# Kernel tuning notes

Hardware: AMD Instinct MI355X
Metric: run time of the kernel (lower is better)

## Reference

```python
import math
import jax, jax.numpy as jnp
import numpy as np

B, S, H, D = 8, 2048, 16, 80
DM = H * D  # 1280 = input_dims


def setup_inputs() -> dict:
    key = jax.random.key(0)
    ks = jax.random.split(key, 10)
    s = 0.02
    return {
        "x": jax.random.normal(ks[0], (B, S, DM), dtype=jnp.float32),
        "Wq": jax.random.normal(ks[1], (DM, DM), dtype=jnp.float32) * s,
        "bq": jnp.zeros((DM,), dtype=jnp.float32),
        "Wk": jax.random.normal(ks[2], (DM, DM), dtype=jnp.float32) * s,
        "bk": jnp.zeros((DM,), dtype=jnp.float32),
        "Wv": jax.random.normal(ks[3], (DM, DM), dtype=jnp.float32) * s,
        "bv": jnp.zeros((DM,), dtype=jnp.float32),
        "Wp": jax.random.normal(ks[4], (DM, DM), dtype=jnp.float32) * s,
        "bp": jnp.zeros((DM,), dtype=jnp.float32),
        "per_dim_scale": jnp.ones((D,), dtype=jnp.float32),
    }


def reference(x, Wq, bq, Wk, bk, Wv, bv, Wp, bp, per_dim_scale):
    # Projections: [B,S,DM] -> [B,S,H,D]
    q = (x @ Wq + bq).reshape(B, S, H, D)
    k = (x @ Wk + bk).reshape(B, S, H, D)
    v = (x @ Wv + bv).reshape(B, S, H, D)
    # Faithful to source: matmul over last two dims of (B,S,H,D) tensors,
    # i.e. scores are [B,S,H,H] -- mixing across HEADS at each position.
    scale = 1.0 / math.sqrt(D)
    attn = jnp.einsum('bshd,bstd->bsht', q, k) * scale  # [B,S,H,H]
    attn = jax.nn.softmax(attn, axis=-1)
    out = jnp.einsum('bsht,bstd->bshd', attn, v)  # [B,S,H,D]
    out = out * per_dim_scale  # broadcast over D
    out = out.reshape(B, S, DM)
    return out @ Wp + bp
```

## Files before the change

kernel.cpp:

```cpp
#include <hip/hip_runtime.h>
#include <hip/hip_bf16.h>

#define M_TOT   16384
#define DMODEL  1280
#define NHEAD   16
#define DHEAD   80
#define NTC     5
#define BK      64
#define NKT     (DMODEL / BK)

typedef __attribute__((ext_vector_type(8))) __bf16 bf16x8;
typedef __attribute__((ext_vector_type(4))) float  f32x4;

__device__ __forceinline__ void gload16(const void* g, void* l) {
  __builtin_amdgcn_global_load_lds(
      (const __attribute__((address_space(1))) void*)g,
      (__attribute__((address_space(3))) void*)l, 16, 0, 0);
}

__device__ __forceinline__ float bf2f(unsigned short u) {
  return __uint_as_float((unsigned)u << 16);
}

__global__ __launch_bounds__(256) void cvt_bf16_kernel(
    const float* __restrict__ x, __hip_bfloat16* __restrict__ y, int n4) {
  int i = blockIdx.x * 256 + threadIdx.x;
  if (i >= n4) return;
  float4 v = ((const float4*)x)[i];
  union { ushort4 u; __hip_bfloat16 h[4]; } o;
  o.h[0] = __float2bfloat16(v.x);
  o.h[1] = __float2bfloat16(v.y);
  o.h[2] = __float2bfloat16(v.z);
  o.h[3] = __float2bfloat16(v.w);
  ((ushort4*)y)[i] = o.u;
}

__global__ __launch_bounds__(256) void transpose_cvt_kernel(
    const float* __restrict__ W0, const float* __restrict__ W1,
    const float* __restrict__ W2, const float* __restrict__ W3,
    __hip_bfloat16* __restrict__ T0, __hip_bfloat16* __restrict__ T1,
    __hip_bfloat16* __restrict__ T2, __hip_bfloat16* __restrict__ T3) {
  const float* W = blockIdx.z == 0 ? W0 : blockIdx.z == 1 ? W1
                 : blockIdx.z == 2 ? W2 : W3;
  __hip_bfloat16* T = blockIdx.z == 0 ? T0 : blockIdx.z == 1 ? T1
                    : blockIdx.z == 2 ? T2 : T3;
  __shared__ float tile[32][33];
  int bx = blockIdx.x * 32, by = blockIdx.y * 32;
  int tx = threadIdx.x, ty = threadIdx.y;
  for (int j = 0; j < 32; j += 8)
    tile[ty + j][tx] = W[(size_t)(by + ty + j) * DMODEL + bx + tx];
  __syncthreads();
  for (int j = 0; j < 32; j += 8)
    T[(size_t)(bx + ty + j) * DMODEL + by + tx] = __float2bfloat16(tile[tx][ty + j]);
}

#define MFMA16(AF, BF, MB)                                                   \
  do {                                                                       \
    _Pragma("unroll")                                                        \
    for (int j_ = 0; j_ < 4; ++j_) {                                         \
      _Pragma("unroll")                                                      \
      for (int n_ = 0; n_ < 4; ++n_)                                         \
        acc[(MB) + j_][n_] = __builtin_amdgcn_mfma_f32_16x16x32_bf16(        \
            AF[j_], BF[n_], acc[(MB) + j_][n_], 0, 0, 0);                    \
    }                                                                        \
  } while (0)

template <bool OUT_BF16>
__global__ __launch_bounds__(512, 2) void gemm_bt_kernel(
    const __hip_bfloat16* __restrict__ A,
    const __hip_bfloat16* __restrict__ Bt0,
    const __hip_bfloat16* __restrict__ Bt1,
    const __hip_bfloat16* __restrict__ Bt2,
    const float* __restrict__ bias0, const float* __restrict__ bias1,
    const float* __restrict__ bias2,
    void* __restrict__ C0, void* __restrict__ C1, void* __restrict__ C2) {
  const int mat   = blockIdx.y / NTC;
  const int ntile = blockIdx.y % NTC;
  const __hip_bfloat16* Bt = mat == 0 ? Bt0 : mat == 1 ? Bt1 : Bt2;
  const float* bias        = mat == 0 ? bias0 : mat == 1 ? bias1 : bias2;
  void* C                  = mat == 0 ? C0 : mat == 1 ? C1 : C2;

  const int bm = blockIdx.x * 256;
  const int bn = ntile * 256;

  __shared__ __align__(16) char SLDS[131072];

  const int tid  = threadIdx.x;
  const int lane = tid & 63;
  const int wid  = tid >> 6;
  const int wm   = (wid >> 2) * 128;
  const int wn   = (wid & 3) * 64;
  const int lrow = lane & 15;
  const int l4   = lane >> 4;

  const int rsub  = lane >> 2;
  const int cswz  = (lane & 3) ^ ((rsub >> 1) & 3);
  const char* gsrc[2][2][2];
#pragma unroll
  for (int i = 0; i < 2; ++i) {
    const int rA = bm + wid * 32 + i * 16 + rsub;
    const int rB = bn + wid * 32 + i * 16 + rsub;
#pragma unroll
    for (int s = 0; s < 2; ++s) {
      gsrc[0][i][s] = (const char*)A  + (size_t)rA * (DMODEL * 2) + s * 64 + cswz * 16;
      gsrc[1][i][s] = (const char*)Bt + (size_t)rB * (DMODEL * 2) + s * 64 + cswz * 16;
    }
  }

  auto issueGroup = [&](int M, int s, int nbuf, size_t koff) {
    char* d = SLDS + M * 65536 + nbuf * 32768 + s * 16384 + wid * 2048;
    gload16(gsrc[M][0][s] + koff, d);
    gload16(gsrc[M][1][s] + koff, d + 1024);
  };

  f32x4 acc[8][4];
#pragma unroll
  for (int i = 0; i < 8; ++i)
#pragma unroll
    for (int j = 0; j < 4; ++j) acc[i][j] = (f32x4){0.f, 0.f, 0.f, 0.f};

  const int swz  = ((l4 ^ ((lrow >> 1) & 3)) << 4);
  const int aOff = (wm + lrow) * 64 + swz;
  const int bOff = 65536 + (wn + lrow) * 64 + swz;

  issueGroup(0, 0, 0, 0);
  issueGroup(1, 0, 0, 0);
  issueGroup(0, 1, 0, 0);
  issueGroup(1, 1, 0, 0);
  asm volatile("s_waitcnt vmcnt(4)" ::: "memory");
  __builtin_amdgcn_s_barrier();

  bf16x8 aFa[4], aFb[4], aFc[4], aFd[4], bF0[4], bF1[4];
#pragma unroll
  for (int j = 0; j < 4; ++j) aFa[j] = *(const bf16x8*)(const void*)(SLDS + aOff + j * 1024);
#pragma unroll
  for (int n = 0; n < 4; ++n) bF0[n] = *(const bf16x8*)(const void*)(SLDS + bOff + n * 1024);
  __builtin_amdgcn_sched_barrier(0);

  for (int t = 0; t < NKT; ++t) {
    const int buf = t & 1, nbuf = buf ^ 1;
    const int b0 = buf << 15;
    const int n0 = nbuf << 15;
    const size_t koff = (size_t)(t + 1) * (BK * 2);
    const bool pf = (t + 1 < NKT);

    __builtin_amdgcn_s_barrier();
#pragma unroll
    for (int j = 0; j < 4; ++j)
      aFb[j] = *(const bf16x8*)(const void*)(SLDS + b0 + aOff + (4 + j) * 1024);
    if (pf) issueGroup(0, 0, nbuf, koff);
    __builtin_amdgcn_sched_barrier(0);
    __builtin_amdgcn_s_setprio(1);
    MFMA16(aFa, bF0, 0);
    __builtin_amdgcn_s_setprio(0);
    __builtin_amdgcn_sched_barrier(0);

    if (pf) asm volatile("s_waitcnt vmcnt(2)" ::: "memory");
    else    asm volatile("s_waitcnt vmcnt(0)" ::: "memory");
    __builtin_amdgcn_s_barrier();
#pragma unroll
    for (int j = 0; j < 4; ++j)
      aFc[j] = *(const bf16x8*)(const void*)(SLDS + b0 + 16384 + aOff + j * 1024);
#pragma unroll
    for (int n = 0; n < 4; ++n)
      bF1[n] = *(const bf16x8*)(const void*)(SLDS + b0 + 16384 + bOff + n * 1024);
    if (pf) issueGroup(1, 0, nbuf, koff);
    __builtin_amdgcn_sched_barrier(0);
    __builtin_amdgcn_s_setprio(1);
    MFMA16(aFb, bF0, 4);
    __builtin_amdgcn_s_setprio(0);
    __builtin_amdgcn_sched_barrier(0);

    __builtin_amdgcn_s_barrier();
#pragma unroll
    for (int j = 0; j < 4; ++j)
      aFd[j] = *(const bf16x8*)(const void*)(SLDS + b0 + 16384 + aOff + (4 + j) * 1024);
    if (pf) issueGroup(0, 1, nbuf, koff);
    __builtin_amdgcn_sched_barrier(0);
    __builtin_amdgcn_s_setprio(1);
    MFMA16(aFc, bF1, 0);
    __builtin_amdgcn_s_setprio(0);
    __builtin_amdgcn_sched_barrier(0);

    if (pf) asm volatile("s_waitcnt vmcnt(2)" ::: "memory");
    __builtin_amdgcn_s_barrier();
    if (pf) {
#pragma unroll
      for (int j = 0; j < 4; ++j)
        aFa[j] = *(const bf16x8*)(const void*)(SLDS + n0 + aOff + j * 1024);
#pragma unroll
      for (int n = 0; n < 4; ++n)
        bF0[n] = *(const bf16x8*)(const void*)(SLDS + n0 + bOff + n * 1024);
      issueGroup(1, 1, nbuf, koff);
    }
    __builtin_amdgcn_sched_barrier(0);
    __builtin_amdgcn_s_setprio(1);
    MFMA16(aFd, bF1, 4);
    __builtin_amdgcn_s_setprio(0);
    __builtin_amdgcn_sched_barrier(0);
  }

  const int rbase = l4 * 4;
#pragma unroll
  for (int mi = 0; mi < 8; ++mi) {
#pragma unroll
    for (int ni = 0; ni < 4; ++ni) {
      const int col = bn + wn + ni * 16 + lrow;
      const float b = bias[col];
#pragma unroll
      for (int r = 0; r < 4; ++r) {
        const int row = bm + wm + mi * 16 + rbase + r;
        const float val = acc[mi][ni][r] + b;
        if (OUT_BF16)
          ((__hip_bfloat16*)C)[(size_t)row * DMODEL + col] = __float2bfloat16(val);
        else
          ((float*)C)[(size_t)row * DMODEL + col] = val;
      }
    }
  }
}

__global__ __launch_bounds__(256) void attn_kernel(
    const __hip_bfloat16* __restrict__ q, const __hip_bfloat16* __restrict__ k,
    const __hip_bfloat16* __restrict__ v, const float* __restrict__ pds,
    __hip_bfloat16* __restrict__ out) {
  const size_t base = (size_t)blockIdx.x * DMODEL;
  __shared__ float qs[16][81], ks[16][81], vs[16][81];
  __shared__ float ps[16][17];
  const int tid = threadIdx.x;

  for (int c = tid; c < 480; c += 256) {
    int matid = c / 160, idx = c - matid * 160;
    int h = idx / 10, d0 = (idx - h * 10) * 8;
    const __hip_bfloat16* src = matid == 0 ? q : matid == 1 ? k : v;
    union { bf16x8 v8; unsigned short u[8]; } uu;
    uu.v8 = *(const bf16x8*)(const void*)(src + base + (size_t)idx * 8);
    float* dst = (matid == 0 ? &qs[0][0] : matid == 1 ? &ks[0][0] : &vs[0][0]) +
                 h * 81 + d0;
#pragma unroll
    for (int j = 0; j < 8; ++j) dst[j] = bf2f(uu.u[j]);
  }
  __syncthreads();

  const int h = tid >> 4, t = tid & 15;
  float s = 0.f;
#pragma unroll
  for (int d = 0; d < DHEAD; ++d) s += qs[h][d] * ks[t][d];
  s *= 0.11180339887498948f;

  float m = s;
#pragma unroll
  for (int off = 8; off; off >>= 1) m = fmaxf(m, __shfl_xor(m, off, 16));
  float e = expf(s - m);
  float sum = e;
#pragma unroll
  for (int off = 8; off; off >>= 1) sum += __shfl_xor(sum, off, 16);
  ps[h][t] = e / sum;
  __syncthreads();

  if (tid < 160) {
    int hh = tid / 10, d0 = (tid - hh * 10) * 8;
    union { bf16x8 v8; unsigned short u[8]; } oo;
#pragma unroll
    for (int j = 0; j < 8; ++j) {
      float o = 0.f;
#pragma unroll
      for (int tt = 0; tt < 16; ++tt) o += ps[hh][tt] * vs[tt][d0 + j];
      o *= pds[d0 + j];
      __hip_bfloat16 hb = __float2bfloat16(o);
      oo.u[j] = *(unsigned short*)&hb;
    }
    *(bf16x8*)(void*)(out + base + (size_t)tid * 8) = oo.v8;
  }
}

extern "C" void kernel_launch(void* const* d_in, const int* in_sizes, int n_in,
                              void* d_out, int out_size, void* d_ws, size_t ws_size,
                              hipStream_t stream) {
  const float* x   = (const float*)d_in[0];
  const float* Wq  = (const float*)d_in[1];
  const float* bq  = (const float*)d_in[2];
  const float* Wk  = (const float*)d_in[3];
  const float* bk  = (const float*)d_in[4];
  const float* Wv  = (const float*)d_in[5];
  const float* bv  = (const float*)d_in[6];
  const float* Wp  = (const float*)d_in[7];
  const float* bp  = (const float*)d_in[8];
  const float* pds = (const float*)d_in[9];
  float* out = (float*)d_out;

  char* ws = (char*)d_ws;
  const size_t ACT = (size_t)M_TOT * DMODEL * 2;
  const size_t WT  = (size_t)DMODEL * DMODEL * 2;
  __hip_bfloat16* xbf = (__hip_bfloat16*)(ws);
  __hip_bfloat16* qbf = (__hip_bfloat16*)(ws + ACT);
  __hip_bfloat16* kbf = (__hip_bfloat16*)(ws + 2 * ACT);
  __hip_bfloat16* vbf = (__hip_bfloat16*)(ws + 3 * ACT);
  __hip_bfloat16* wtq = (__hip_bfloat16*)(ws + 4 * ACT);
  __hip_bfloat16* wtk = (__hip_bfloat16*)(ws + 4 * ACT + WT);
  __hip_bfloat16* wtv = (__hip_bfloat16*)(ws + 4 * ACT + 2 * WT);
  __hip_bfloat16* wtp = (__hip_bfloat16*)(ws + 4 * ACT + 3 * WT);
  __hip_bfloat16* attnbf = xbf;

  {
    int n4 = (M_TOT * DMODEL) / 4;
    cvt_bf16_kernel<<<n4 / 256, 256, 0, stream>>>(x, xbf, n4);
  }
  {
    dim3 g(DMODEL / 32, DMODEL / 32, 4), b(32, 8);
    transpose_cvt_kernel<<<g, b, 0, stream>>>(Wq, Wk, Wv, Wp, wtq, wtk, wtv, wtp);
  }
  {
    dim3 g(M_TOT / 256, 3 * NTC);
    gemm_bt_kernel<true><<<g, 512, 0, stream>>>(
        xbf, wtq, wtk, wtv, bq, bk, bv, (void*)qbf, (void*)kbf, (void*)vbf);
  }
  attn_kernel<<<M_TOT, 256, 0, stream>>>(qbf, kbf, vbf, pds, attnbf);
  {
    dim3 g(M_TOT / 256, NTC);
    gemm_bt_kernel<false><<<g, 512, 0, stream>>>(
        attnbf, wtp, wtp, wtp, bp, bp, bp, (void*)out, (void*)out, (void*)out);
  }
}
```

Baseline: 349.4 us.

## Add 128x128 tiled output-projection GEMM and spread attention PV work across all threads

Adds a dedicated 128x128-tile GEMM kernel with 256 threads and double-buffered LDS loads for the output projection. It replaces the 256-row tile used before, which launched only 64x5 blocks. The new kernel is meant to raise block count and occupancy so the CUs are better filled. The attention kernel's P·V stage now uses all 256 threads with 5 outputs each instead of 160 threads with 8. That trades the 16-byte vector stores for scalar bf16 stores.

```diff
diff --git a/kernel.cpp b/kernel.cpp
--- a/kernel.cpp
+++ b/kernel.cpp
@@ -220,6 +220,114 @@
   }
 }
 
+__global__ __launch_bounds__(256, 2) void gemm_bt128_kernel(
+    const __hip_bfloat16* __restrict__ A,
+    const __hip_bfloat16* __restrict__ Bt,
+    const float* __restrict__ bias,
+    float* __restrict__ C) {
+  const int bm = blockIdx.x * 128;
+  const int bn = blockIdx.y * 128;
+
+  __shared__ __align__(16) char SLDS[65536];
+
+  const int tid  = threadIdx.x;
+  const int lane = tid & 63;
+  const int wid  = tid >> 6;
+  const int wm   = (wid >> 1) * 64;
+  const int wn   = (wid & 1) * 64;
+  const int lrow = lane & 15;
+  const int l4   = lane >> 4;
+
+  const int rsub  = lane >> 2;
+  const int cswz  = (lane & 3) ^ ((rsub >> 1) & 3);
+  const char* gsrc[2][2][2];
+#pragma unroll
+  for (int i = 0; i < 2; ++i) {
+    const int rA = bm + wid * 32 + i * 16 + rsub;
+    const int rB = bn + wid * 32 + i * 16 + rsub;
+#pragma unroll
+    for (int s = 0; s < 2; ++s) {
+      gsrc[0][i][s] = (const char*)A  + (size_t)rA * (DMODEL * 2) + s * 64 + cswz * 16;
+      gsrc[1][i][s] = (const char*)Bt + (size_t)rB * (DMODEL * 2) + s * 64 + cswz * 16;
+    }
+  }
+
+  auto issueGroup = [&](int M, int s, int nbuf, size_t koff) {
+    char* d = SLDS + M * 32768 + nbuf * 16384 + s * 8192 + wid * 2048;
+    gload16(gsrc[M][0][s] + koff, d);
+    gload16(gsrc[M][1][s] + koff, d + 1024);
+  };
+
+  f32x4 acc[4][4];
+#pragma unroll
+  for (int i = 0; i < 4; ++i)
+#pragma unroll
+    for (int j = 0; j < 4; ++j) acc[i][j] = (f32x4){0.f, 0.f, 0.f, 0.f};
+
+  const int swz  = ((l4 ^ ((lrow >> 1) & 3)) << 4);
+  const int aOff = (wm + lrow) * 64 + swz;
+  const int bOff = 32768 + (wn + lrow) * 64 + swz;
+
+  issueGroup(0, 0, 0, 0);
+  issueGroup(1, 0, 0, 0);
+  issueGroup(0, 1, 0, 0);
+  issueGroup(1, 1, 0, 0);
+
+  for (int t = 0; t < NKT; ++t) {
+    const int buf = t & 1, nbuf = buf ^ 1;
+    const int b0 = buf << 14;
+    const size_t koff = (size_t)(t + 1) * (BK * 2);
+    const bool pf = (t + 1 < NKT);
+
+    asm volatile("s_waitcnt vmcnt(4)" ::: "memory");
+    __builtin_amdgcn_s_barrier();
+    bf16x8 aF[4], bF[4];
+#pragma unroll
+    for (int j = 0; j < 4; ++j)
+      aF[j] = *(const bf16x8*)(const void*)(SLDS + b0 + aOff + j * 1024);
+#pragma unroll
+    for (int n = 0; n < 4; ++n)
+      bF[n] = *(const bf16x8*)(const void*)(SLDS + b0 + bOff + n * 1024);
+    if (pf) { issueGroup(0, 0, nbuf, koff); issueGroup(1, 0, nbuf, koff); }
+    __builtin_amdgcn_sched_barrier(0);
+    __builtin_amdgcn_s_setprio(1);
+    MFMA16(aF, bF, 0);
+    __builtin_amdgcn_s_setprio(0);
+    __builtin_amdgcn_sched_barrier(0);
+
+    if (pf) asm volatile("s_waitcnt vmcnt(4)" ::: "memory");
+    else    asm volatile("s_waitcnt vmcnt(0)" ::: "memory");
+    __builtin_amdgcn_s_barrier();
+#pragma unroll
+    for (int j = 0; j < 4; ++j)
+      aF[j] = *(const bf16x8*)(const void*)(SLDS + b0 + 8192 + aOff + j * 1024);
+#pragma unroll
+    for (int n = 0; n < 4; ++n)
+      bF[n] = *(const bf16x8*)(const void*)(SLDS + b0 + 8192 + bOff + n * 1024);
+    if (pf) { issueGroup(0, 1, nbuf, koff); issueGroup(1, 1, nbuf, koff); }
+    __builtin_amdgcn_sched_barrier(0);
+    __builtin_amdgcn_s_setprio(1);
+    MFMA16(aF, bF, 0);
+    __builtin_amdgcn_s_setprio(0);
+    __builtin_amdgcn_sched_barrier(0);
+  }
+
+  const int rbase = l4 * 4;
+#pragma unroll
+  for (int mi = 0; mi < 4; ++mi) {
+#pragma unroll
+    for (int ni = 0; ni < 4; ++ni) {
+      const int col = bn + wn + ni * 16 + lrow;
+      const float b = bias[col];
+#pragma unroll
+      for (int r = 0; r < 4; ++r) {
+        const int row = bm + wm + mi * 16 + rbase + r;
+        C[(size_t)row * DMODEL + col] = acc[mi][ni][r] + b;
+      }
+    }
+  }
+}
+
 __global__ __launch_bounds__(256) void attn_kernel(
     const __hip_bfloat16* __restrict__ q, const __hip_bfloat16* __restrict__ k,
     const __hip_bfloat16* __restrict__ v, const float* __restrict__ pds,
@@ -258,19 +366,21 @@
   ps[h][t] = e / sum;
   __syncthreads();
 
-  if (tid < 160) {
-    int hh = tid / 10, d0 = (tid - hh * 10) * 8;
-    union { bf16x8 v8; unsigned short u[8]; } oo;
-#pragma unroll
-    for (int j = 0; j < 8; ++j) {
-      float o = 0.f;
-#pragma unroll
-      for (int tt = 0; tt < 16; ++tt) o += ps[hh][tt] * vs[tt][d0 + j];
-      o *= pds[d0 + j];
-      __hip_bfloat16 hb = __float2bfloat16(o);
-      oo.u[j] = *(unsigned short*)&hb;
-    }
-    *(bf16x8*)(void*)(out + base + (size_t)tid * 8) = oo.v8;
+  {
+    const int hh   = tid >> 4;
+    const int dloc = (tid & 15) * 5;
+    float o[5];
+#pragma unroll
+    for (int j = 0; j < 5; ++j) o[j] = 0.f;
+#pragma unroll
+    for (int tt = 0; tt < 16; ++tt) {
+      const float p = ps[hh][tt];
+#pragma unroll
+      for (int j = 0; j < 5; ++j) o[j] += p * vs[tt][dloc + j];
+    }
+    __hip_bfloat16* ob = out + base + (size_t)hh * DHEAD + dloc;
+#pragma unroll
+    for (int j = 0; j < 5; ++j) ob[j] = __float2bfloat16(o[j] * pds[dloc + j]);
   }
 }
 
@@ -317,8 +427,7 @@
   }
   attn_kernel<<<M_TOT, 256, 0, stream>>>(qbf, kbf, vbf, pds, attnbf);
   {
-    dim3 g(M_TOT / 256, NTC);
-    gemm_bt_kernel<false><<<g, 512, 0, stream>>>(
-        attnbf, wtp, wtp, wtp, bp, bp, bp, (void*)out, (void*)out, (void*)out);
-  }
-}
+    dim3 g(M_TOT / 128, DMODEL / 128);
+    gemm_bt128_kernel<<<g, 256, 0, stream>>>(attnbf, wtp, bp, out);
+  }
+}
```

Result: faster. 316.7 us (-9.4%).
